# Optimization experiments

Hardware: AMD Instinct MI355X
Metric: run time of the kernel (lower is better)

The kernel has to match this reference:

```python
import jax, jax.numpy as jnp
import numpy as np

D = 512
EXPAND = 2
INNER = D * EXPAND          # 1024
DT_RANK = 32                # ceil(512/16)
D_STATE = 16
D_CONV = 4
B, L = 4, 1024


def setup_inputs() -> dict:
    key = jax.random.key(0)
    ks = jax.random.split(key, 9)
    s = lambda fan: 1.0 / np.sqrt(fan)
    x = jax.random.normal(ks[0], (B, L, D), dtype=jnp.float32)
    W_in = jax.random.normal(ks[1], (2 * INNER, D), dtype=jnp.float32) * s(D)
    conv_w = jax.random.normal(ks[2], (INNER, 1, D_CONV), dtype=jnp.float32) * s(D_CONV)
    conv_b = jax.random.normal(ks[3], (INNER,), dtype=jnp.float32) * 0.01
    W_x = jax.random.normal(ks[4], (DT_RANK + 2 * D_STATE, INNER), dtype=jnp.float32) * s(INNER)
    W_dt = jax.random.normal(ks[5], (INNER, DT_RANK), dtype=jnp.float32) * s(DT_RANK)
    b_dt = jax.random.normal(ks[6], (INNER,), dtype=jnp.float32) * 0.01
    # A_log init: log(arange(1..d_state)) broadcast over inner channels
    A_log = jnp.broadcast_to(jnp.log(jnp.arange(1, D_STATE + 1, dtype=jnp.float32))[None, :], (INNER, D_STATE))
    D_ssm = jnp.ones((INNER,), dtype=jnp.float32)
    W_out = jax.random.normal(ks[7], (D, INNER), dtype=jnp.float32) * s(INNER)
    return dict(x=x, W_in=W_in, conv_w=conv_w, conv_b=conv_b, W_x=W_x,
                W_dt=W_dt, b_dt=b_dt, A_log=A_log, D_ssm=D_ssm, W_out=W_out)


def _mamba_fwd(x, W_in, conv_w, conv_b, W_x, W_dt, b_dt, A_log, D_ssm, W_out):
    # in_proj then split into x-branch and gate z: [B,L,inner] each
    xz = x @ W_in.T
    xi, z = jnp.split(xz, 2, axis=-1)
    # depthwise causal conv1d: pad (d_conv-1) on the left == torch's pad-both + slice[:L]
    xc = jax.lax.conv_general_dilated(
        xi.transpose(0, 2, 1), conv_w, window_strides=(1,),
        padding=[(D_CONV - 1, 0)], feature_group_count=INNER,
        dimension_numbers=("NCH", "OIH", "NCH"))
    xc = jax.nn.silu((xc + conv_b[None, :, None]).transpose(0, 2, 1))  # [B,L,inner]
    # input-dependent SSM params
    proj = xc @ W_x.T
    dt, Bs, Cs = jnp.split(proj, [DT_RANK, DT_RANK + D_STATE], axis=-1)
    dt = jax.nn.softplus(dt @ W_dt.T + b_dt)          # [B,L,inner]
    A = -jnp.exp(A_log)                                # [inner,n]
    dA = jnp.exp(jnp.einsum('bld,dn->bldn', dt, A))    # [B,L,inner,n]
    dB = jnp.einsum('bld,bln->bldn', dt, Bs)           # [B,L,inner,n]

    def step(h, t):
        dA_t, dB_t, xc_t, C_t = t                      # [B,inner,n],[B,inner,n],[B,inner],[B,n]
        h = h * dA_t + dB_t * xc_t[..., None]
        y = jnp.einsum('bdn,bn->bd', h, C_t)
        return h, y

    h0 = jnp.zeros((x.shape[0], INNER, D_STATE), dtype=x.dtype)
    xs = (dA.transpose(1, 0, 2, 3), dB.transpose(1, 0, 2, 3),
          xc.transpose(1, 0, 2), Cs.transpose(1, 0, 2))
    _, ys = jax.lax.scan(step, h0, xs)                 # ys: [L,B,inner]
    ys = ys.transpose(1, 0, 2)
    return ((ys + xc * D_ssm) * jax.nn.silu(z)) @ W_out.T


def reference(x, W_in, conv_w, conv_b, W_x, W_dt, b_dt, A_log, D_ssm, W_out):
    return _mamba_fwd(x, W_in, conv_w, conv_b, W_x, W_dt, b_dt, A_log, D_ssm, W_out)
```

## Files before the change

### kernel.cpp

```cpp
#include <hip/hip_runtime.h>
#include <math.h>

#define D_MODEL 512
#define INNER   1024
#define DT_RANK 32
#define BATCH   4
#define SEQ     1024
#define BL      (BATCH*SEQ)
#define NCHUNK  32
#define TCHUNK  32

typedef __attribute__((ext_vector_type(8))) short  bf16x8;
typedef __attribute__((ext_vector_type(4))) float  f32x4;

__device__ __forceinline__ float silu_f(float x) { return x / (1.0f + __expf(-x)); }

__device__ __forceinline__ unsigned short f2bf(float f) {
    unsigned u = __float_as_uint(f);
    u += 0x7FFF + ((u >> 16) & 1);
    return (unsigned short)(u >> 16);
}
__device__ __forceinline__ float bf2f(unsigned short h) {
    return __uint_as_float(((unsigned)h) << 16);
}

__device__ __forceinline__ void gld_lds16(const void* g, void* l) {
    __builtin_amdgcn_global_load_lds(
        (const __attribute__((address_space(1))) unsigned int*)g,
        (__attribute__((address_space(3))) unsigned int*)l, 16, 0, 0);
}

__global__ __launch_bounds__(256)
void pack_all(const float* __restrict__ x,     const float* __restrict__ W_in,
              const float* __restrict__ W_x,   const float* __restrict__ W_dt,
              const float* __restrict__ W_out,
              unsigned short* __restrict__ apk1, unsigned short* __restrict__ bpk1,
              unsigned short* __restrict__ bpk2, unsigned short* __restrict__ bpk3,
              unsigned short* __restrict__ bpk4)
{
    int idx = blockIdx.x * 256 + threadIdx.x;
    if (idx < 2097152) {
        apk1[idx] = f2bf(x[idx]);
        return;
    }
    idx -= 2097152;
    if (idx < 1048576) {
        int m = idx >> 9, k = idx & 511;
        float a = W_in[idx];
        unsigned short hi = f2bf(a);
        size_t o = (size_t)m * 1024;
        bpk1[o + k] = hi; bpk1[o + 512 + k] = f2bf(a - bf2f(hi));
        return;
    }
    idx -= 1048576;
    if (idx < 65536) {
        int m = idx >> 10, k = idx & 1023;
        float a = W_x[idx];
        unsigned short hi = f2bf(a);
        size_t o = (size_t)m * 2048;
        bpk2[o + k] = hi; bpk2[o + 1024 + k] = f2bf(a - bf2f(hi));
        return;
    }
    idx -= 65536;
    if (idx < 32768) {
        int m = idx >> 5, k = idx & 31;
        float a = W_dt[idx];
        unsigned short hi = f2bf(a);
        size_t o = (size_t)m * 128;
        bpk3[o + k] = hi; bpk3[o + 32 + k] = 0;
        bpk3[o + 64 + k] = f2bf(a - bf2f(hi)); bpk3[o + 96 + k] = 0;
        return;
    }
    idx -= 32768;
    if (idx < 524288) {
        bpk4[idx] = f2bf(W_out[idx]);
    }
}

template<int BM, int BN, int EPI, int XS, int SK>
__global__ __launch_bounds__(256)
void gemm_mfma(const unsigned short* __restrict__ Ap,
               const unsigned short* __restrict__ Bp,
               float* __restrict__ C, int ldc, int K, int KS,
               const float* __restrict__ bias)
{
    constexpr int FM = BM / 32;
    constexpr int FN = BN / 32;
    constexpr int AH = 0;
    constexpr int AL = BM * 64;
    constexpr int BH_ = 2 * BM * 64;
    constexpr int BL_ = (2 * BM + BN) * 64;
    __shared__ __align__(16) unsigned short S[(2 * BM + 2 * BN) * 64];

    const int tid  = threadIdx.x;
    const int wave = tid >> 6, lane = tid & 63;
    const int wr = wave >> 1, wc = wave & 1;
    const int crow = lane >> 3, cslot = lane & 7;
    const int K2 = 2 * K;

    int bx, by;
    if (XS) {
        int f   = blockIdx.y * gridDim.x + blockIdx.x;
        int bh  = gridDim.y >> 3;
        int xcd = f & 7, i = f >> 3;
        by = xcd * bh + (i % bh);
        bx = i / bh;
    } else { bx = blockIdx.x; by = blockIdx.y; }

    const int brow = by * BM, bcol = bx * BN;
    int kbeg = 0, kend = K;
    float* Cp = C;
    if (SK) {
        kbeg = blockIdx.z * KS; kend = kbeg + KS;
        Cp = C + (size_t)blockIdx.z * (size_t)gridDim.y * BM * ldc;
    }

    f32x4 acc[FM][FN];
    #pragma unroll
    for (int i = 0; i < FM; ++i)
        #pragma unroll
        for (int j = 0; j < FN; ++j) acc[i][j] = f32x4{0.f, 0.f, 0.f, 0.f};

    for (int k0 = kbeg; k0 < kend; k0 += 64) {
        #pragma unroll
        for (int c = wave; c < BM / 8; c += 4) {
            int row = c * 8 + crow;
            int ls  = cslot ^ (row & 7);
            const unsigned short* src = Ap + (size_t)(brow + row) * K2 + k0 + ls * 8;
            gld_lds16(src,     (char*)(S + AH) + c * 1024);
            gld_lds16(src + K, (char*)(S + AL) + c * 1024);
        }
        #pragma unroll
        for (int c = wave; c < BN / 8; c += 4) {
            int row = c * 8 + crow;
            int ls  = cslot ^ (row & 7);
            const unsigned short* src = Bp + (size_t)(bcol + row) * K2 + k0 + ls * 8;
            gld_lds16(src,     (char*)(S + BH_) + c * 1024);
            gld_lds16(src + K, (char*)(S + BL_) + c * 1024);
        }
        __syncthreads();

        #pragma unroll
        for (int ks = 0; ks < 2; ++ks) {
            bf16x8 ah[FM], al[FM], bh[FN], bl[FN];
            #pragma unroll
            for (int i = 0; i < FM; ++i) {
                int row = wr * (BM / 2) + i * 16 + (lane & 15);
                int ph  = (ks * 4 + (lane >> 4)) ^ (row & 7);
                ah[i] = *(const bf16x8*)((const char*)(S + AH) + row * 128 + ph * 16);
                al[i] = *(const bf16x8*)((const char*)(S + AL) + row * 128 + ph * 16);
            }
            #pragma unroll
            for (int j = 0; j < FN; ++j) {
                int row = wc * (BN / 2) + j * 16 + (lane & 15);
                int ph  = (ks * 4 + (lane >> 4)) ^ (row & 7);
                bh[j] = *(const bf16x8*)((const char*)(S + BH_) + row * 128 + ph * 16);
                bl[j] = *(const bf16x8*)((const char*)(S + BL_) + row * 128 + ph * 16);
            }
            #pragma unroll
            for (int i = 0; i < FM; ++i)
                #pragma unroll
                for (int j = 0; j < FN; ++j) {
                    acc[i][j] = __builtin_amdgcn_mfma_f32_16x16x32_bf16(
                        ah[i], bh[j], acc[i][j], 0, 0, 0);
                    acc[i][j] = __builtin_amdgcn_mfma_f32_16x16x32_bf16(
                        ah[i], bl[j], acc[i][j], 0, 0, 0);
                    acc[i][j] = __builtin_amdgcn_mfma_f32_16x16x32_bf16(
                        al[i], bh[j], acc[i][j], 0, 0, 0);
                }
        }
        __syncthreads();
    }

    const int cb = lane & 15, rb = (lane >> 4) * 4;
    #pragma unroll
    for (int i = 0; i < FM; ++i) {
        #pragma unroll
        for (int j = 0; j < FN; ++j) {
            int col = bcol + wc * (BN / 2) + j * 16 + cb;
            float bv = (EPI == 1) ? bias[col] : 0.f;
            #pragma unroll
            for (int q = 0; q < 4; ++q) {
                int row = brow + wr * (BM / 2) + i * 16 + rb + q;
                float v = acc[i][j][q];
                if (EPI == 1) { v += bv; v = (v > 20.f) ? v : log1pf(__expf(v)); }
                Cp[(size_t)row * ldc + col] = v;
            }
        }
    }
}

template<int BM, int BN>
__global__ __launch_bounds__(256)
void gemm_a1b2(const unsigned short* __restrict__ Ap,
               const unsigned short* __restrict__ Bp,
               float* __restrict__ C, int ldc, int K)
{
    constexpr int FM = BM / 32;
    constexpr int FN = BN / 32;
    constexpr int AH = 0;
    constexpr int BH_ = BM * 64;
    constexpr int BL_ = (BM + BN) * 64;
    __shared__ __align__(16) unsigned short S[(BM + 2 * BN) * 64];

    const int tid  = threadIdx.x;
    const int wave = tid >> 6, lane = tid & 63;
    const int wr = wave >> 1, wc = wave & 1;
    const int crow = lane >> 3, cslot = lane & 7;
    const int K2 = 2 * K;

    int f   = blockIdx.y * gridDim.x + blockIdx.x;
    int bh  = gridDim.y >> 3;
    int xcd = f & 7, i0 = f >> 3;
    const int by = xcd * bh + (i0 % bh);
    const int bx = i0 / bh;
    const int brow = by * BM, bcol = bx * BN;

    f32x4 acc[FM][FN];
    #pragma unroll
    for (int i = 0; i < FM; ++i)
        #pragma unroll
        for (int j = 0; j < FN; ++j) acc[i][j] = f32x4{0.f, 0.f, 0.f, 0.f};

    for (int k0 = 0; k0 < K; k0 += 64) {
        #pragma unroll
        for (int c = wave; c < BM / 8; c += 4) {
            int row = c * 8 + crow;
            int ls  = cslot ^ (row & 7);
            gld_lds16(Ap + (size_t)(brow + row) * K + k0 + ls * 8,
                      (char*)(S + AH) + c * 1024);
        }
        #pragma unroll
        for (int c = wave; c < BN / 8; c += 4) {
            int row = c * 8 + crow;
            int ls  = cslot ^ (row & 7);
            const unsigned short* src = Bp + (size_t)(bcol + row) * K2 + k0 + ls * 8;
            gld_lds16(src,     (char*)(S + BH_) + c * 1024);
            gld_lds16(src + K, (char*)(S + BL_) + c * 1024);
        }
        __syncthreads();

        #pragma unroll
        for (int ks = 0; ks < 2; ++ks) {
            bf16x8 ah[FM], bh2[FN], bl2[FN];
            #pragma unroll
            for (int i = 0; i < FM; ++i) {
                int row = wr * (BM / 2) + i * 16 + (lane & 15);
                int ph  = (ks * 4 + (lane >> 4)) ^ (row & 7);
                ah[i] = *(const bf16x8*)((const char*)(S + AH) + row * 128 + ph * 16);
            }
            #pragma unroll
            for (int j = 0; j < FN; ++j) {
                int row = wc * (BN / 2) + j * 16 + (lane & 15);
                int ph  = (ks * 4 + (lane >> 4)) ^ (row & 7);
                bh2[j] = *(const bf16x8*)((const char*)(S + BH_) + row * 128 + ph * 16);
                bl2[j] = *(const bf16x8*)((const char*)(S + BL_) + row * 128 + ph * 16);
            }
            #pragma unroll
            for (int i = 0; i < FM; ++i)
                #pragma unroll
                for (int j = 0; j < FN; ++j) {
                    acc[i][j] = __builtin_amdgcn_mfma_f32_16x16x32_bf16(
                        ah[i], bh2[j], acc[i][j], 0, 0, 0);
                    acc[i][j] = __builtin_amdgcn_mfma_f32_16x16x32_bf16(
                        ah[i], bl2[j], acc[i][j], 0, 0, 0);
                }
        }
        __syncthreads();
    }

    const int cb = lane & 15, rb = (lane >> 4) * 4;
    #pragma unroll
    for (int i = 0; i < FM; ++i)
        #pragma unroll
        for (int j = 0; j < FN; ++j) {
            int col = bcol + wc * (BN / 2) + j * 16 + cb;
            #pragma unroll
            for (int q = 0; q < 4; ++q) {
                int row = brow + wr * (BM / 2) + i * 16 + rb + q;
                C[(size_t)row * ldc + col] = acc[i][j][q];
            }
        }
}

template<int BM, int BN>
__global__ __launch_bounds__(256)
void gemm_bf(const unsigned short* __restrict__ Ap,
             const unsigned short* __restrict__ Bp,
             float* __restrict__ C, int ldc, int K)
{
    constexpr int FM = BM / 32;
    constexpr int FN = BN / 32;
    __shared__ __align__(16) unsigned short S[(BM + BN) * 64];
    constexpr int BO = BM * 64;

    const int tid  = threadIdx.x;
    const int wave = tid >> 6, lane = tid & 63;
    const int wr = wave >> 1, wc = wave & 1;
    const int crow = lane >> 3, cslot = lane & 7;

    int f   = blockIdx.y * gridDim.x + blockIdx.x;
    int bh  = gridDim.y >> 3;
    int xcd = f & 7, i0 = f >> 3;
    const int by = xcd * bh + (i0 % bh);
    const int bx = i0 / bh;
    const int brow = by * BM, bcol = bx * BN;

    f32x4 acc[FM][FN];
    #pragma unroll
    for (int i = 0; i < FM; ++i)
        #pragma unroll
        for (int j = 0; j < FN; ++j) acc[i][j] = f32x4{0.f, 0.f, 0.f, 0.f};

    for (int k0 = 0; k0 < K; k0 += 64) {
        #pragma unroll
        for (int c = wave; c < BM / 8; c += 4) {
            int row = c * 8 + crow;
            int ls  = cslot ^ (row & 7);
            gld_lds16(Ap + (size_t)(brow + row) * K + k0 + ls * 8,
                      (char*)S + c * 1024);
        }
        #pragma unroll
        for (int c = wave; c < BN / 8; c += 4) {
            int row = c * 8 + crow;
            int ls  = cslot ^ (row & 7);
            gld_lds16(Bp + (size_t)(bcol + row) * K + k0 + ls * 8,
                      (char*)(S + BO) + c * 1024);
        }
        __syncthreads();

        #pragma unroll
        for (int ks = 0; ks < 2; ++ks) {
            bf16x8 af[FM], bf2[FN];
            #pragma unroll
            for (int i = 0; i < FM; ++i) {
                int row = wr * (BM / 2) + i * 16 + (lane & 15);
                int ph  = (ks * 4 + (lane >> 4)) ^ (row & 7);
                af[i] = *(const bf16x8*)((const char*)S + row * 128 + ph * 16);
            }
            #pragma unroll
            for (int j = 0; j < FN; ++j) {
                int row = wc * (BN / 2) + j * 16 + (lane & 15);
                int ph  = (ks * 4 + (lane >> 4)) ^ (row & 7);
                bf2[j] = *(const bf16x8*)((const char*)(S + BO) + row * 128 + ph * 16);
            }
            #pragma unroll
            for (int i = 0; i < FM; ++i)
                #pragma unroll
                for (int j = 0; j < FN; ++j)
                    acc[i][j] = __builtin_amdgcn_mfma_f32_16x16x32_bf16(
                        af[i], bf2[j], acc[i][j], 0, 0, 0);
        }
        __syncthreads();
    }

    const int cb = lane & 15, rb = (lane >> 4) * 4;
    #pragma unroll
    for (int i = 0; i < FM; ++i)
        #pragma unroll
        for (int j = 0; j < FN; ++j) {
            int col = bcol + wc * (BN / 2) + j * 16 + cb;
            #pragma unroll
            for (int q = 0; q < 4; ++q) {
                int row = brow + wr * (BM / 2) + i * 16 + rb + q;
                C[(size_t)row * ldc + col] = acc[i][j][q];
            }
        }
}

__global__ __launch_bounds__(256)
void reduce4_pack(const float* __restrict__ part,
                  float* __restrict__ proj,
                  unsigned short* __restrict__ apk3)
{
    int idx = blockIdx.x * 256 + threadIdx.x;
    if (idx >= BL * 64) return;
    const int n = BL * 64;
    float v = part[idx] + part[n + idx] + part[2 * n + idx] + part[3 * n + idx];
    proj[idx] = v;
    int m = idx >> 6, k = idx & 63;
    size_t o = (size_t)m * 128;
    if (k < 32) {
        unsigned short hi = f2bf(v);
        apk3[o + k]      = hi;
        apk3[o + 64 + k] = f2bf(v - bf2f(hi));
    } else {
        apk3[o + k]      = 0;
        apk3[o + 64 + k] = 0;
    }
}

__global__ __launch_bounds__(256)
void conv_silu_kernel(const float* __restrict__ xz,
                      const float* __restrict__ cw,
                      const float* __restrict__ cb,
                      float* __restrict__ xc,
                      unsigned short* __restrict__ apk2)
{
    int idx = blockIdx.x * 256 + threadIdx.x;
    int d  = idx & (INNER - 1);
    int bt = idx >> 10;
    int t  = bt & (SEQ - 1);

    float w0 = cw[d * 4 + 0], w1 = cw[d * 4 + 1];
    float w2 = cw[d * 4 + 2], w3 = cw[d * 4 + 3];

    float x0 = (t >= 3) ? xz[(size_t)(bt - 3) * 2048 + d] : 0.0f;
    float x1 = (t >= 2) ? xz[(size_t)(bt - 2) * 2048 + d] : 0.0f;
    float x2 = (t >= 1) ? xz[(size_t)(bt - 1) * 2048 + d] : 0.0f;
    float x3 =            xz[(size_t)(bt    ) * 2048 + d];

    float acc = cb[d] + x0 * w0 + x1 * w1 + x2 * w2 + x3 * w3;
    float v = silu_f(acc);
    xc[idx] = v;
    unsigned short hi = f2bf(v);
    apk2[(size_t)bt * 2048 + d] = hi;
    apk2[(size_t)bt * 2048 + 1024 + d] = f2bf(v - bf2f(hi));
}


__global__ __launch_bounds__(256)
void ssm_pass1(const float* __restrict__ dt,
               const float* __restrict__ xc,
               const float* __restrict__ proj,
               float* __restrict__ Pbuf,
               float* __restrict__ qbuf)
{
    const int tid  = threadIdx.x;
    const int dblk = blockIdx.x & 3;
    const int c    = (blockIdx.x >> 2) & (NCHUNK - 1);
    const int b    = blockIdx.x >> 7;
    const int d    = dblk * 256 + tid;

    __shared__ float sB[TCHUNK][16];
    const size_t base = (size_t)b * SEQ + c * TCHUNK;

    for (int s = tid; s < TCHUNK * 16; s += 256) {
        int tt = s >> 4, nn = s & 15;
        sB[tt][nn] = proj[(base + tt) * 64 + 32 + nn];
    }
    __syncthreads();

    float h[16];
    #pragma unroll
    for (int n = 0; n < 16; ++n) h[n] = 0.f;
    float S = 0.f;

    #pragma unroll 2
    for (int tt = 0; tt < TCHUNK; ++tt) {
        size_t row = base + tt;
        float dtv = dt[row * INNER + d];
        float xv  = xc[row * INNER + d];
        S += dtv;
        float r = __expf(-dtv), r2 = r * r;
        float po = r, pe = r2, dtx = dtv * xv;
        #pragma unroll
        for (int m = 0; m < 8; ++m) {
            h[2*m]   = fmaf(h[2*m],   po, dtx * sB[tt][2*m]);
            h[2*m+1] = fmaf(h[2*m+1], pe, dtx * sB[tt][2*m+1]);
            po *= r2; pe *= r2;
        }
    }

    float rS = __expf(-S), rS2 = rS * rS;
    float po = rS, pe = rS2;
    float P[16];
    #pragma unroll
    for (int m = 0; m < 8; ++m) { P[2*m] = po; P[2*m+1] = pe; po *= rS2; pe *= rS2; }

    size_t o = (((size_t)b * NCHUNK + c) * INNER + d) * 16;
    #pragma unroll
    for (int v = 0; v < 4; ++v) {
        *(f32x4*)(Pbuf + o + 4*v) = f32x4{P[4*v], P[4*v+1], P[4*v+2], P[4*v+3]};
        *(f32x4*)(qbuf + o + 4*v) = f32x4{h[4*v], h[4*v+1], h[4*v+2], h[4*v+3]};
    }
}

__global__ __launch_bounds__(256)
void ssm_pass2(const float* __restrict__ Pbuf,
               const float* __restrict__ qbuf,
               float* __restrict__ hstart)
{
    int idx = blockIdx.x * 256 + threadIdx.x;
    int n = idx & 15, d = (idx >> 4) & (INNER - 1), b = idx >> 14;

    float h = 0.f;
    #pragma unroll
    for (int c = 0; c < NCHUNK; ++c) {
        size_t o = (((size_t)b * NCHUNK + c) * INNER + d) * 16 + n;
        hstart[o] = h;
        h = fmaf(Pbuf[o], h, qbuf[o]);
    }
}

__global__ __launch_bounds__(256)
void ssm_pass3(const float* __restrict__ dt,
               const float* __restrict__ xc,
               const float* __restrict__ proj,
               const float* __restrict__ D_ssm,
               const float* __restrict__ xz,
               const float* __restrict__ hstart,
               unsigned short* __restrict__ apk4)
{
    const int tid  = threadIdx.x;
    const int dblk = blockIdx.x & 3;
    const int c    = (blockIdx.x >> 2) & (NCHUNK - 1);
    const int b    = blockIdx.x >> 7;
    const int d    = dblk * 256 + tid;

    __shared__ float sBC[TCHUNK][32];
    const size_t base = (size_t)b * SEQ + c * TCHUNK;

    for (int s = tid; s < TCHUNK * 32; s += 256) {
        int tt = s >> 5, nn = s & 31;
        sBC[tt][nn] = proj[(base + tt) * 64 + 32 + nn];
    }
    __syncthreads();

    float h[16];
    size_t ho = (((size_t)b * NCHUNK + c) * INNER + d) * 16;
    #pragma unroll
    for (int v = 0; v < 4; ++v) {
        f32x4 hv = *(const f32x4*)(hstart + ho + 4*v);
        h[4*v] = hv[0]; h[4*v+1] = hv[1]; h[4*v+2] = hv[2]; h[4*v+3] = hv[3];
    }
    const float dssm = D_ssm[d];

    #pragma unroll 2
    for (int tt = 0; tt < TCHUNK; ++tt) {
        size_t row = base + tt;
        float dtv = dt[row * INNER + d];
        float xv  = xc[row * INNER + d];
        float r = __expf(-dtv), r2 = r * r;
        float po = r, pe = r2, dtx = dtv * xv;
        float y0 = 0.f, y1 = 0.f;
        #pragma unroll
        for (int m = 0; m < 8; ++m) {
            h[2*m]   = fmaf(h[2*m],   po, dtx * sBC[tt][2*m]);
            h[2*m+1] = fmaf(h[2*m+1], pe, dtx * sBC[tt][2*m+1]);
            y0 = fmaf(h[2*m],   sBC[tt][16 + 2*m],   y0);
            y1 = fmaf(h[2*m+1], sBC[tt][16 + 2*m+1], y1);
            po *= r2; pe *= r2;
        }
        float zv = xz[row * 2048 + INNER + d];
        float v  = (y0 + y1 + xv * dssm) * silu_f(zv);
        apk4[row * 1024 + d] = f2bf(v);
    }
}

extern "C" void kernel_launch(void* const* d_in, const int* in_sizes, int n_in,
                              void* d_out, int out_size, void* d_ws, size_t ws_size,
                              hipStream_t stream)
{
    const float* x      = (const float*)d_in[0];
    const float* W_in   = (const float*)d_in[1];
    const float* conv_w = (const float*)d_in[2];
    const float* conv_b = (const float*)d_in[3];
    const float* W_x    = (const float*)d_in[4];
    const float* W_dt   = (const float*)d_in[5];
    const float* b_dt   = (const float*)d_in[6];
    const float* D_ssm  = (const float*)d_in[8];
    const float* W_out  = (const float*)d_in[9];
    float* out = (float*)d_out;

    char* W = (char*)d_ws;
    float* xz            = (float*)(W + 0);
    float* xc            = (float*)(W + 33554432);
    float* proj          = (float*)(W + 50331648);
    float* dtb           = (float*)(W + 51380224);
    unsigned short* apk2 = (unsigned short*)(W + 68157440);
    unsigned short* apk4 = (unsigned short*)(W + 84934656);
    unsigned short* apk1 = (unsigned short*)(W + 101711872);
    unsigned short* bpk1 = (unsigned short*)(W + 110100480);
    unsigned short* bpk2 = (unsigned short*)(W + 114294784);
    unsigned short* bpk3 = (unsigned short*)(W + 114556928);
    unsigned short* bpk4 = (unsigned short*)(W + 114819072);
    unsigned short* apk3 = (unsigned short*)(W + 116916224);
    float* g2part        = (float*)(W + 117964800);
    float* Pbuf   = (float*)(W + 68157440);
    float* qbuf   = (float*)(W + 76546048);
    float* hstart = (float*)(W + 101711872);

    pack_all<<<(3768320 + 255) / 256, 256, 0, stream>>>(
        x, W_in, W_x, W_dt, W_out, apk1, bpk1, bpk2, bpk3, bpk4);

    gemm_a1b2<128, 128><<<dim3(16, 32), 256, 0, stream>>>(apk1, bpk1, xz, 2048, 512);

    conv_silu_kernel<<<(BL * INNER) / 256, 256, 0, stream>>>(xz, conv_w, conv_b, xc, apk2);

    gemm_mfma<64, 64, 0, 0, 1><<<dim3(1, 64, 4), 256, 0, stream>>>(
        apk2, bpk2, g2part, 64, 1024, 256, nullptr);
    reduce4_pack<<<(BL * 64 + 255) / 256, 256, 0, stream>>>(g2part, proj, apk3);

    gemm_mfma<128, 128, 1, 1, 0><<<dim3(8, 32), 256, 0, stream>>>(
        apk3, bpk3, dtb, 1024, 64, 0, b_dt);

    ssm_pass1<<<BATCH * NCHUNK * (INNER / 256), 256, 0, stream>>>(
        dtb, xc, proj, Pbuf, qbuf);
    ssm_pass2<<<(BATCH * INNER * 16) / 256, 256, 0, stream>>>(Pbuf, qbuf, hstart);
    ssm_pass3<<<BATCH * NCHUNK * (INNER / 256), 256, 0, stream>>>(
        dtb, xc, proj, D_ssm, xz, hstart, apk4);

    gemm_bf<64, 64><<<dim3(8, 64), 256, 0, stream>>>(apk4, bpk4, out, 512, 1024);
}
```

Measured before the change: 142.3 us.

## Replace dt projection GEMM with fp32 FMA kernel and widen in_proj GEMM to 512 threads

The dt projection (K=32) previously needed bf16 hi/lo packing of W_dt and proj plus an MFMA GEMM. It is now a direct fp32 FMA kernel that reads proj and W_dt and applies bias and softplus. This drops the bpk3/apk3 packing work and one pass through packed buffers. Separately, the in_proj GEMM now runs 8 waves per 128x128 tile instead of 4, halving per-wave M fragments to raise parallelism. The trade-off is more threads sharing the same LDS tile per block. The dt kernel also reloads each 32-float W_dt row per block rather than reusing it from a tensor-core tile.

```diff
diff --git a/kernel.cpp b/kernel.cpp
--- a/kernel.cpp
+++ b/kernel.cpp
@@ -32,11 +32,9 @@
 
 __global__ __launch_bounds__(256)
 void pack_all(const float* __restrict__ x,     const float* __restrict__ W_in,
-              const float* __restrict__ W_x,   const float* __restrict__ W_dt,
-              const float* __restrict__ W_out,
+              const float* __restrict__ W_x,   const float* __restrict__ W_out,
               unsigned short* __restrict__ apk1, unsigned short* __restrict__ bpk1,
-              unsigned short* __restrict__ bpk2, unsigned short* __restrict__ bpk3,
-              unsigned short* __restrict__ bpk4)
+              unsigned short* __restrict__ bpk2, unsigned short* __restrict__ bpk4)
 {
     int idx = blockIdx.x * 256 + threadIdx.x;
     if (idx < 2097152) {
@@ -62,16 +60,6 @@
         return;
     }
     idx -= 65536;
-    if (idx < 32768) {
-        int m = idx >> 5, k = idx & 31;
-        float a = W_dt[idx];
-        unsigned short hi = f2bf(a);
-        size_t o = (size_t)m * 128;
-        bpk3[o + k] = hi; bpk3[o + 32 + k] = 0;
-        bpk3[o + 64 + k] = f2bf(a - bf2f(hi)); bpk3[o + 96 + k] = 0;
-        return;
-    }
-    idx -= 32768;
     if (idx < 524288) {
         bpk4[idx] = f2bf(W_out[idx]);
     }
@@ -191,12 +179,12 @@
 }
 
 template<int BM, int BN>
-__global__ __launch_bounds__(256)
+__global__ __launch_bounds__(512)
 void gemm_a1b2(const unsigned short* __restrict__ Ap,
                const unsigned short* __restrict__ Bp,
                float* __restrict__ C, int ldc, int K)
 {
-    constexpr int FM = BM / 32;
+    constexpr int FM = BM / 64;
     constexpr int FN = BN / 32;
     constexpr int AH = 0;
     constexpr int BH_ = BM * 64;
@@ -224,14 +212,14 @@
 
     for (int k0 = 0; k0 < K; k0 += 64) {
         #pragma unroll
-        for (int c = wave; c < BM / 8; c += 4) {
+        for (int c = wave; c < BM / 8; c += 8) {
             int row = c * 8 + crow;
             int ls  = cslot ^ (row & 7);
             gld_lds16(Ap + (size_t)(brow + row) * K + k0 + ls * 8,
                       (char*)(S + AH) + c * 1024);
         }
         #pragma unroll
-        for (int c = wave; c < BN / 8; c += 4) {
+        for (int c = wave; c < BN / 8; c += 8) {
             int row = c * 8 + crow;
             int ls  = cslot ^ (row & 7);
             const unsigned short* src = Bp + (size_t)(bcol + row) * K2 + k0 + ls * 8;
@@ -245,7 +233,7 @@
             bf16x8 ah[FM], bh2[FN], bl2[FN];
             #pragma unroll
             for (int i = 0; i < FM; ++i) {
-                int row = wr * (BM / 2) + i * 16 + (lane & 15);
+                int row = wr * (BM / 4) + i * 16 + (lane & 15);
                 int ph  = (ks * 4 + (lane >> 4)) ^ (row & 7);
                 ah[i] = *(const bf16x8*)((const char*)(S + AH) + row * 128 + ph * 16);
             }
@@ -277,7 +265,7 @@
             int col = bcol + wc * (BN / 2) + j * 16 + cb;
             #pragma unroll
             for (int q = 0; q < 4; ++q) {
-                int row = brow + wr * (BM / 2) + i * 16 + rb + q;
+                int row = brow + wr * (BM / 4) + i * 16 + rb + q;
                 C[(size_t)row * ldc + col] = acc[i][j][q];
             }
         }
@@ -369,24 +357,43 @@
 }
 
 __global__ __launch_bounds__(256)
-void reduce4_pack(const float* __restrict__ part,
-                  float* __restrict__ proj,
-                  unsigned short* __restrict__ apk3)
+void reduce4(const float* __restrict__ part, float* __restrict__ proj)
 {
     int idx = blockIdx.x * 256 + threadIdx.x;
     if (idx >= BL * 64) return;
     const int n = BL * 64;
-    float v = part[idx] + part[n + idx] + part[2 * n + idx] + part[3 * n + idx];
-    proj[idx] = v;
-    int m = idx >> 6, k = idx & 63;
-    size_t o = (size_t)m * 128;
-    if (k < 32) {
-        unsigned short hi = f2bf(v);
-        apk3[o + k]      = hi;
-        apk3[o + 64 + k] = f2bf(v - bf2f(hi));
-    } else {
-        apk3[o + k]      = 0;
-        apk3[o + 64 + k] = 0;
+    proj[idx] = part[idx] + part[n + idx] + part[2 * n + idx] + part[3 * n + idx];
+}
+
+__global__ __launch_bounds__(256)
+void dt_kernel(const float* __restrict__ proj,
+               const float* __restrict__ W_dt,
+               const float* __restrict__ b_dt,
+               float* __restrict__ dtb)
+{
+    const int mb = blockIdx.x * 8;
+    const int t  = threadIdx.x;
+    __shared__ float sp[8][32];
+    {
+        int s = t;
+        sp[s >> 5][s & 31] = proj[(size_t)(mb + (s >> 5)) * 64 + (s & 31)];
+    }
+    __syncthreads();
+
+    #pragma unroll
+    for (int j = 0; j < 4; ++j) {
+        int d = t + 256 * j;
+        float b = b_dt[d];
+        float w[32];
+        #pragma unroll
+        for (int k = 0; k < 32; ++k) w[k] = W_dt[d * 32 + k];
+        #pragma unroll
+        for (int m = 0; m < 8; ++m) {
+            float a = b;
+            #pragma unroll
+            for (int k = 0; k < 32; ++k) a = fmaf(sp[m][k], w[k], a);
+            dtb[(size_t)(mb + m) * INNER + d] = (a > 20.f) ? a : log1pf(__expf(a));
+        }
     }
 }
 
@@ -573,27 +580,24 @@
     unsigned short* apk1 = (unsigned short*)(W + 101711872);
     unsigned short* bpk1 = (unsigned short*)(W + 110100480);
     unsigned short* bpk2 = (unsigned short*)(W + 114294784);
-    unsigned short* bpk3 = (unsigned short*)(W + 114556928);
     unsigned short* bpk4 = (unsigned short*)(W + 114819072);
-    unsigned short* apk3 = (unsigned short*)(W + 116916224);
     float* g2part        = (float*)(W + 117964800);
     float* Pbuf   = (float*)(W + 68157440);
     float* qbuf   = (float*)(W + 76546048);
     float* hstart = (float*)(W + 101711872);
 
-    pack_all<<<(3768320 + 255) / 256, 256, 0, stream>>>(
-        x, W_in, W_x, W_dt, W_out, apk1, bpk1, bpk2, bpk3, bpk4);
-
-    gemm_a1b2<128, 128><<<dim3(16, 32), 256, 0, stream>>>(apk1, bpk1, xz, 2048, 512);
+    pack_all<<<(3735552 + 255) / 256, 256, 0, stream>>>(
+        x, W_in, W_x, W_out, apk1, bpk1, bpk2, bpk4);
+
+    gemm_a1b2<128, 128><<<dim3(16, 32), 512, 0, stream>>>(apk1, bpk1, xz, 2048, 512);
 
     conv_silu_kernel<<<(BL * INNER) / 256, 256, 0, stream>>>(xz, conv_w, conv_b, xc, apk2);
 
     gemm_mfma<64, 64, 0, 0, 1><<<dim3(1, 64, 4), 256, 0, stream>>>(
         apk2, bpk2, g2part, 64, 1024, 256, nullptr);
-    reduce4_pack<<<(BL * 64 + 255) / 256, 256, 0, stream>>>(g2part, proj, apk3);
-
-    gemm_mfma<128, 128, 1, 1, 0><<<dim3(8, 32), 256, 0, stream>>>(
-        apk3, bpk3, dtb, 1024, 64, 0, b_dt);
+    reduce4<<<(BL * 64 + 255) / 256, 256, 0, stream>>>(g2part, proj);
+
+    dt_kernel<<<BL / 8, 256, 0, stream>>>(proj, W_dt, b_dt, dtb);
 
     ssm_pass1<<<BATCH * NCHUNK * (INNER / 256), 256, 0, stream>>>(
         dtb, xc, proj, Pbuf, qbuf);
```

New measurement: 140.0 us. No clear change (-1.6%).
